# Kernel tuning notes

Measured on AMD Instinct MI355X. Metric: run time of the kernel, lower is better.

## Reference

```python
import jax, jax.numpy as jnp
import numpy as np

BATCH, PAST_N, HID, FEAT = 256, 512, 512, 1
INIT_MULT = 0.01  # ones * 0.01 initial state (perturb_init=False / eval mode)


def setup_inputs() -> dict:
    key = jax.random.key(0)
    ks = jax.random.split(key, 8)
    s = 1.0 / np.sqrt(HID)
    return {
        "input_seq": jax.random.normal(ks[0], (BATCH, PAST_N, FEAT), dtype=jnp.float32),
        "future_n": 64,
        "W_ih": jax.random.uniform(ks[1], (4 * HID, FEAT), minval=-s, maxval=s, dtype=jnp.float32),
        "W_hh": jax.random.uniform(ks[2], (4 * HID, HID), minval=-s, maxval=s, dtype=jnp.float32),
        "b_ih": jax.random.uniform(ks[3], (4 * HID,), minval=-s, maxval=s, dtype=jnp.float32),
        "b_hh": jax.random.uniform(ks[4], (4 * HID,), minval=-s, maxval=s, dtype=jnp.float32),
        "W_dec": jax.random.uniform(ks[5], (FEAT, HID), minval=-s, maxval=s, dtype=jnp.float32),
        "b_dec": jax.random.uniform(ks[6], (FEAT,), minval=-s, maxval=s, dtype=jnp.float32),
    }


def _lstm_cell(x, h, c, W_ih, W_hh, b_ih, b_hh):
    # PyTorch LSTMCell: gates ordered (i, f, g, o)
    gates = x @ W_ih.T + b_ih + h @ W_hh.T + b_hh  # [B, 4H]
    i, f, g, o = jnp.split(gates, 4, axis=-1)
    c_new = jax.nn.sigmoid(f) * c + jax.nn.sigmoid(i) * jnp.tanh(g)
    h_new = jax.nn.sigmoid(o) * jnp.tanh(c_new)
    return h_new, c_new


def reference(input_seq, future_n, W_ih, W_hh, b_ih, b_hh, W_dec, b_dec):
    B, T, _ = input_seq.shape
    h0 = jnp.full((B, HID), INIT_MULT, dtype=input_seq.dtype)
    c0 = jnp.full((B, HID), INIT_MULT, dtype=input_seq.dtype)

    xs = jnp.swapaxes(input_seq, 0, 1)  # [T, B, F]

    def past_step(carry, x_t):
        h, c = carry
        h, c = _lstm_cell(x_t, h, c, W_ih, W_hh, b_ih, b_hh)
        return (h, c), h

    (h, c), past_h = jax.lax.scan(past_step, (h0, c0), xs)  # past_h: [T, B, H]

    def future_step(carry, _):
        h, c = carry
        x_t = h @ W_dec.T + b_dec  # decode hidden -> next input, [B, F]
        h, c = _lstm_cell(x_t, h, c, W_ih, W_hh, b_ih, b_hh)
        return (h, c), h

    _, fut_h = jax.lax.scan(future_step, (h, c), None, length=future_n)  # [F_n, B, H]

    all_h = jnp.concatenate([past_h, fut_h], axis=0)  # [T+F_n, B, H]
    all_h = jnp.swapaxes(all_h, 0, 1)  # [B, T+F_n, H]
    return all_h @ W_dec.T + b_dec  # [B, T+F_n, 1]
```

## Files before the change

kernel.cpp:

```cpp
#include <hip/hip_runtime.h>
#include <hip/hip_fp16.h>


#define TPAST 512
#define TTOT  576
#define HIDN  512
#define BW    16
#define HW    64
#define NGRP  8
#define NWG   128
#define NTHR  512
#define HSTR  520
#define GSTR  261
#define BATCHN 256

typedef _Float16 half8   __attribute__((ext_vector_type(8)));
typedef _Float16 half2v  __attribute__((ext_vector_type(2)));
typedef float    float4v __attribute__((ext_vector_type(4)));
typedef int      int4v   __attribute__((ext_vector_type(4)));

__device__ __forceinline__ float fast_exp(float x) {
    return __builtin_amdgcn_exp2f(x * 1.44269504f);
}
__device__ __forceinline__ float fast_sigmoid(float x) {
    return __builtin_amdgcn_rcpf(1.0f + fast_exp(-x));
}
__device__ __forceinline__ float fast_tanh(float x) {
    return 1.0f - 2.0f * __builtin_amdgcn_rcpf(fast_exp(2.0f * x) + 1.0f);
}

__device__ __forceinline__ void ld32_sys(const void* p, int4v& a, int4v& b) {
    asm volatile("global_load_dwordx4 %0, %2, off sc0 sc1\n\t"
                 "global_load_dwordx4 %1, %2, off offset:16 sc0 sc1\n\t"
                 "s_waitcnt vmcnt(0)"
                 : "=v"(a), "=v"(b) : "v"(p) : "memory");
}
__device__ __forceinline__ void drain_vm() {
    asm volatile("s_waitcnt vmcnt(0)" ::: "memory");
}

__global__ __launch_bounds__(NTHR, 1)
void lstm_forecast_kernel(const float* __restrict__ xseq,
                          const float* __restrict__ Wih,
                          const float* __restrict__ Whh,
                          const float* __restrict__ bih,
                          const float* __restrict__ bhh,
                          const float* __restrict__ Wdec,
                          const float* __restrict__ bdec,
                          float* __restrict__ out,
                          unsigned int* __restrict__ flagbase,
                          unsigned int* __restrict__ hbuf)
{
    __shared__ _Float16 hcur[BW * HSTR];
    __shared__ float    gates[BW * GSTR];
    __shared__ float    wdecs[HIDN];
    __shared__ float    xcur[BW];

    const int tid  = threadIdx.x;
    const int bb   = blockIdx.x & 15;
    const int gb   = blockIdx.x >> 4;
    const int lane = tid & 63;
    const int wave = tid >> 6;
    const int m    = lane & 15;
    const int q    = lane >> 4;

    half8 Wf[2][16];
    {
        #pragma unroll
        for (int cbi = 0; cbi < 2; ++cbi) {
            const int col = (2 * wave + cbi) * 16 + m;
            const int gt  = col >> 6;
            const int jl  = col & 63;
            const float* wr = Whh + (size_t)(gt * HIDN + gb * HW + jl) * HIDN;
            #pragma unroll
            for (int kk = 0; kk < 16; ++kk) {
                const int k0 = kk * 32 + q * 8;
                float4v u = *(const float4v*)(wr + k0);
                float4v v = *(const float4v*)(wr + k0 + 4);
                half8 h;
                h[0] = (_Float16)u[0]; h[1] = (_Float16)u[1];
                h[2] = (_Float16)u[2]; h[3] = (_Float16)u[3];
                h[4] = (_Float16)v[0]; h[5] = (_Float16)v[1];
                h[6] = (_Float16)v[2]; h[7] = (_Float16)v[3];
                Wf[cbi][kk] = h;
            }
        }
    }

    const int eb = tid >> 5;
    const int jj = tid & 31;
    const int j0 = 2 * jj;
    float wih_r[2][4], bsum_r[2][4];
    #pragma unroll
    for (int p = 0; p < 2; ++p) {
        const int jg = gb * HW + j0 + p;
        #pragma unroll
        for (int gt = 0; gt < 4; ++gt) {
            const int r = gt * HIDN + jg;
            wih_r[p][gt]  = Wih[r];
            bsum_r[p][gt] = bih[r] + bhh[r];
        }
    }
    const float bdecv = bdec[0];
    float c0 = 0.01f, c1 = 0.01f;

    {
        const _Float16 hinit = (_Float16)0.01f;
        for (int i = tid; i < BW * HSTR; i += NTHR) hcur[i] = hinit;
        wdecs[tid] = Wdec[tid];
        if (tid < BW) xcur[tid] = xseq[(bb * BW + tid) * TPAST + 0];
    }
    __syncthreads();

    unsigned int* gflags = flagbase + bb * 16;
    const int bglob_e = bb * BW + eb;

    for (int t = 0; t < TTOT; ++t) {
        float4v acc0 = {0.f, 0.f, 0.f, 0.f};
        float4v acc1 = {0.f, 0.f, 0.f, 0.f};
        const _Float16* arow = hcur + m * HSTR + q * 8;
        #pragma unroll
        for (int kk = 0; kk < 16; ++kk) {
            half8 af = *(const half8*)(arow + kk * 32);
            acc0 = __builtin_amdgcn_mfma_f32_16x16x32_f16(af, Wf[0][kk], acc0, 0, 0, 0);
            acc1 = __builtin_amdgcn_mfma_f32_16x16x32_f16(af, Wf[1][kk], acc1, 0, 0, 0);
        }
        {
            const int colbase = wave * 32;
            #pragma unroll
            for (int r = 0; r < 4; ++r) {
                gates[(q * 4 + r) * GSTR + colbase +      m] = acc0[r];
                gates[(q * 4 + r) * GSTR + colbase + 16 + m] = acc1[r];
            }
        }
        const int tn = t + 1;
        float xq = 0.f;
        if (tn < TPAST && tid < BW) xq = xseq[(bb * BW + tid) * TPAST + tn];

        __syncthreads();

        {
            const float xc = xcur[eb];
            const float* grow = gates + eb * GSTR;

            float gi = grow[       j0] + xc * wih_r[0][0] + bsum_r[0][0];
            float gf = grow[ 64  + j0] + xc * wih_r[0][1] + bsum_r[0][1];
            float gg = grow[128  + j0] + xc * wih_r[0][2] + bsum_r[0][2];
            float go = grow[192  + j0] + xc * wih_r[0][3] + bsum_r[0][3];
            c0 = fast_sigmoid(gf) * c0 + fast_sigmoid(gi) * fast_tanh(gg);
            const float h0 = fast_sigmoid(go) * fast_tanh(c0);

            gi = grow[       j0 + 1] + xc * wih_r[1][0] + bsum_r[1][0];
            gf = grow[ 64  + j0 + 1] + xc * wih_r[1][1] + bsum_r[1][1];
            gg = grow[128  + j0 + 1] + xc * wih_r[1][2] + bsum_r[1][2];
            go = grow[192  + j0 + 1] + xc * wih_r[1][3] + bsum_r[1][3];
            c1 = fast_sigmoid(gf) * c1 + fast_sigmoid(gi) * fast_tanh(gg);
            const float h1 = fast_sigmoid(go) * fast_tanh(c1);

            half2v hp; hp[0] = (_Float16)h0; hp[1] = (_Float16)h1;
            const unsigned int bits = __builtin_bit_cast(unsigned int, hp);
            unsigned int* hdst = hbuf
                + (size_t)((tn & 1) * BATCHN + bglob_e) * (HIDN / 2)
                + gb * (HW / 2) + jj;
            __hip_atomic_store(hdst, bits, __ATOMIC_RELAXED,
                               __HIP_MEMORY_SCOPE_AGENT);
        }

        drain_vm();
        __syncthreads();

        const unsigned int target = (unsigned int)tn;
        if (tid == 0)
            __hip_atomic_store(gflags + gb, target, __ATOMIC_RELAXED,
                               __HIP_MEMORY_SCOPE_AGENT);
        {
            const unsigned int* slot = gflags + (lane & 7);
            int guard = 0;
            for (;;) {
                const unsigned int v = __hip_atomic_load(
                    slot, __ATOMIC_RELAXED, __HIP_MEMORY_SCOPE_AGENT);
                if (__ballot(v >= target) == ~0ull) break;
                __builtin_amdgcn_s_sleep(1);
                if (++guard > (1 << 22)) break;
            }
        }
        __builtin_amdgcn_sched_barrier(0);

        {
            const int p1 = tn & 1;
            const char* hsrc = (const char*)hbuf
                + ((size_t)(p1 * BATCHN + bb * BW)) * (HIDN * 2);
            const int row = 2 * wave + (lane >> 5);
            const int cb  = (lane & 31) * 32;
            int4v a, b;
            ld32_sys(hsrc + row * (HIDN * 2) + cb, a, b);
            _Float16* dst = hcur + row * HSTR + (lane & 31) * 16;
            *(int4v*)(dst)     = a;
            *(int4v*)(dst + 8) = b;
        }
        __syncthreads();

        if (wave < 2) {
            const int brow = 2 * gb + wave;
            const _Float16* hr = hcur + brow * HSTR + lane * 8;
            const float*    wr = wdecs + lane * 8;
            half8 hv = *(const half8*)hr;
            float dx = 0.f;
            #pragma unroll
            for (int e = 0; e < 8; ++e) dx += (float)hv[e] * wr[e];
            dx += __shfl_down(dx, 32);
            dx += __shfl_down(dx, 16);
            dx += __shfl_down(dx, 8);
            dx += __shfl_down(dx, 4);
            dx += __shfl_down(dx, 2);
            dx += __shfl_down(dx, 1);
            if (lane == 0)
                out[(bb * BW + brow) * TTOT + t] = dx + bdecv;
        }
        if (tn >= TPAST) {
            const _Float16* hr = hcur + eb * HSTR + jj * 16;
            const float*    wr = wdecs + jj * 16;
            float dx = 0.f;
            #pragma unroll
            for (int u = 0; u < 2; ++u) {
                half8 hv = *(const half8*)(hr + u * 8);
                #pragma unroll
                for (int e = 0; e < 8; ++e)
                    dx += (float)hv[e] * wr[u * 8 + e];
            }
            dx += __shfl_down(dx, 16);
            dx += __shfl_down(dx, 8);
            dx += __shfl_down(dx, 4);
            dx += __shfl_down(dx, 2);
            dx += __shfl_down(dx, 1);
            if ((lane & 31) == 0) xcur[eb] = dx + bdecv;
        } else {
            if (tid < BW) xcur[tid] = xq;
        }
    }
}

extern "C" void kernel_launch(void* const* d_in, const int* in_sizes, int n_in,
                              void* d_out, int out_size, void* d_ws, size_t ws_size,
                              hipStream_t stream) {
    (void)in_sizes; (void)n_in; (void)ws_size; (void)out_size;
    const float* xseq = (const float*)d_in[0];
    const float* Wih  = (const float*)d_in[2];
    const float* Whh  = (const float*)d_in[3];
    const float* bih  = (const float*)d_in[4];
    const float* bhh  = (const float*)d_in[5];
    const float* Wdec = (const float*)d_in[6];
    const float* bdec = (const float*)d_in[7];
    float* out = (float*)d_out;

    unsigned int* flags = (unsigned int*)d_ws;
    unsigned int* hbuf  = (unsigned int*)((char*)d_ws + 8192);

    hipMemsetAsync(d_ws, 0, 8192, stream);
    lstm_forecast_kernel<<<dim3(NWG), dim3(NTHR), 0, stream>>>(
        xseq, Wih, Whh, bih, bhh, Wdec, bdec, out, flags, hbuf);
}
```

Before: 1.662 ms.

## Use per-wave byte flags for grid sync and fuse decoder dot into h load

Replaces the per-workgroup flag, which needed a __syncthreads before one thread published it, with per-wave byte flags. Each wave publishes its own flag right after draining its stores and polls all 64 peer flags without sleeping, so one block-wide barrier per step goes away. The decoder dot product is now computed from the registers just loaded from the global h buffer, using Wdec held in registers, which removes a separate LDS pass and the shared Wdec array. The trade-offs are more flag traffic from 64 waves spinning, a wrapping 8-bit counter compared modulo 256, and a smaller spin guard.

```diff
diff --git a/kernel.cpp b/kernel.cpp
--- a/kernel.cpp
+++ b/kernel.cpp
@@ -35,6 +35,15 @@
                  "s_waitcnt vmcnt(0)"
                  : "=v"(a), "=v"(b) : "v"(p) : "memory");
 }
+__device__ __forceinline__ void st_byte_agent(unsigned char* p, unsigned int v) {
+    asm volatile("global_store_byte %0, %1, off sc1" :: "v"(p), "v"(v) : "memory");
+}
+__device__ __forceinline__ unsigned int ld_ubyte_agent(const unsigned char* p) {
+    unsigned int v;
+    asm volatile("global_load_ubyte %0, %1, off sc1\n\ts_waitcnt vmcnt(0)"
+                 : "=v"(v) : "v"(p) : "memory");
+    return v;
+}
 __device__ __forceinline__ void drain_vm() {
     asm volatile("s_waitcnt vmcnt(0)" ::: "memory");
 }
@@ -48,12 +57,11 @@
                           const float* __restrict__ Wdec,
                           const float* __restrict__ bdec,
                           float* __restrict__ out,
-                          unsigned int* __restrict__ flagbase,
+                          unsigned char* __restrict__ flagbase,
                           unsigned int* __restrict__ hbuf)
 {
     __shared__ _Float16 hcur[BW * HSTR];
     __shared__ float    gates[BW * GSTR];
-    __shared__ float    wdecs[HIDN];
     __shared__ float    xcur[BW];
 
     const int tid  = threadIdx.x;
@@ -101,21 +109,28 @@
             bsum_r[p][gt] = bih[r] + bhh[r];
         }
     }
+    float wdreg[16];
+    #pragma unroll
+    for (int e = 0; e < 16; ++e) wdreg[e] = Wdec[(lane & 31) * 16 + e];
     const float bdecv = bdec[0];
     float c0 = 0.01f, c1 = 0.01f;
 
     {
         const _Float16 hinit = (_Float16)0.01f;
         for (int i = tid; i < BW * HSTR; i += NTHR) hcur[i] = hinit;
-        wdecs[tid] = Wdec[tid];
         if (tid < BW) xcur[tid] = xseq[(bb * BW + tid) * TPAST + 0];
     }
     __syncthreads();
 
-    unsigned int* gflags = flagbase + bb * 16;
+    unsigned char* gflags = flagbase + bb * 128;
+    const int myidx = gb * 8 + wave;
     const int bglob_e = bb * BW + eb;
 
     for (int t = 0; t < TTOT; ++t) {
+        const int tn = t + 1;
+        float xq = 0.f;
+        if (tn < TPAST && tid < BW) xq = xseq[(bb * BW + tid) * TPAST + tn];
+
         float4v acc0 = {0.f, 0.f, 0.f, 0.f};
         float4v acc1 = {0.f, 0.f, 0.f, 0.f};
         const _Float16* arow = hcur + m * HSTR + q * 8;
@@ -133,10 +148,6 @@
                 gates[(q * 4 + r) * GSTR + colbase + 16 + m] = acc1[r];
             }
         }
-        const int tn = t + 1;
-        float xq = 0.f;
-        if (tn < TPAST && tid < BW) xq = xseq[(bb * BW + tid) * TPAST + tn];
-
         __syncthreads();
 
         {
@@ -167,76 +178,62 @@
         }
 
         drain_vm();
-        __syncthreads();
-
-        const unsigned int target = (unsigned int)tn;
-        if (tid == 0)
-            __hip_atomic_store(gflags + gb, target, __ATOMIC_RELAXED,
-                               __HIP_MEMORY_SCOPE_AGENT);
-        {
-            const unsigned int* slot = gflags + (lane & 7);
+        const unsigned int target8 = (unsigned int)tn & 0xffu;
+        if (lane == 0)
+            st_byte_agent(gflags + myidx, target8);
+        {
             int guard = 0;
             for (;;) {
-                const unsigned int v = __hip_atomic_load(
-                    slot, __ATOMIC_RELAXED, __HIP_MEMORY_SCOPE_AGENT);
-                if (__ballot(v >= target) == ~0ull) break;
-                __builtin_amdgcn_s_sleep(1);
-                if (++guard > (1 << 22)) break;
+                const unsigned int v = ld_ubyte_agent(gflags + lane);
+                const bool ok = (lane == myidx) || (((v - target8) & 0xffu) < 2u);
+                if (__ballot(ok) == ~0ull) break;
+                if (++guard > (1 << 19)) break;
             }
         }
         __builtin_amdgcn_sched_barrier(0);
 
+        int4v ra, rb;
         {
             const int p1 = tn & 1;
             const char* hsrc = (const char*)hbuf
                 + ((size_t)(p1 * BATCHN + bb * BW)) * (HIDN * 2);
             const int row = 2 * wave + (lane >> 5);
             const int cb  = (lane & 31) * 32;
-            int4v a, b;
-            ld32_sys(hsrc + row * (HIDN * 2) + cb, a, b);
+            ld32_sys(hsrc + row * (HIDN * 2) + cb, ra, rb);
             _Float16* dst = hcur + row * HSTR + (lane & 31) * 16;
-            *(int4v*)(dst)     = a;
-            *(int4v*)(dst + 8) = b;
+            *(int4v*)(dst)     = ra;
+            *(int4v*)(dst + 8) = rb;
+        }
+
+        {
+            const half8 ha = __builtin_bit_cast(half8, ra);
+            const half8 hb = __builtin_bit_cast(half8, rb);
+            float d = 0.f;
+            #pragma unroll
+            for (int e = 0; e < 8; ++e) d += (float)ha[e] * wdreg[e];
+            #pragma unroll
+            for (int e = 0; e < 8; ++e) d += (float)hb[e] * wdreg[8 + e];
+            d += __shfl_down(d, 16);
+            d += __shfl_down(d, 8);
+            d += __shfl_down(d, 4);
+            d += __shfl_down(d, 2);
+            d += __shfl_down(d, 1);
+            const float val = d + bdecv;
+
+            if (wave == gb) {
+                if (lane == 0)
+                    out[(bb * BW + 2 * gb    ) * TTOT + t] = val;
+                else if (lane == 32)
+                    out[(bb * BW + 2 * gb + 1) * TTOT + t] = val;
+            }
+            if (tn >= TPAST) {
+                if (lane == 0)       xcur[2 * wave    ] = val;
+                else if (lane == 32) xcur[2 * wave + 1] = val;
+            } else {
+                if (tid < BW) xcur[tid] = xq;
+            }
         }
         __syncthreads();
-
-        if (wave < 2) {
-            const int brow = 2 * gb + wave;
-            const _Float16* hr = hcur + brow * HSTR + lane * 8;
-            const float*    wr = wdecs + lane * 8;
-            half8 hv = *(const half8*)hr;
-            float dx = 0.f;
-            #pragma unroll
-            for (int e = 0; e < 8; ++e) dx += (float)hv[e] * wr[e];
-            dx += __shfl_down(dx, 32);
-            dx += __shfl_down(dx, 16);
-            dx += __shfl_down(dx, 8);
-            dx += __shfl_down(dx, 4);
-            dx += __shfl_down(dx, 2);
-            dx += __shfl_down(dx, 1);
-            if (lane == 0)
-                out[(bb * BW + brow) * TTOT + t] = dx + bdecv;
-        }
-        if (tn >= TPAST) {
-            const _Float16* hr = hcur + eb * HSTR + jj * 16;
-            const float*    wr = wdecs + jj * 16;
-            float dx = 0.f;
-            #pragma unroll
-            for (int u = 0; u < 2; ++u) {
-                half8 hv = *(const half8*)(hr + u * 8);
-                #pragma unroll
-                for (int e = 0; e < 8; ++e)
-                    dx += (float)hv[e] * wr[u * 8 + e];
-            }
-            dx += __shfl_down(dx, 16);
-            dx += __shfl_down(dx, 8);
-            dx += __shfl_down(dx, 4);
-            dx += __shfl_down(dx, 2);
-            dx += __shfl_down(dx, 1);
-            if ((lane & 31) == 0) xcur[eb] = dx + bdecv;
-        } else {
-            if (tid < BW) xcur[tid] = xq;
-        }
     }
 }
 
@@ -253,8 +250,8 @@
     const float* bdec = (const float*)d_in[7];
     float* out = (float*)d_out;
 
-    unsigned int* flags = (unsigned int*)d_ws;
-    unsigned int* hbuf  = (unsigned int*)((char*)d_ws + 8192);
+    unsigned char* flags = (unsigned char*)d_ws;
+    unsigned int*  hbuf  = (unsigned int*)((char*)d_ws + 8192);
 
     hipMemsetAsync(d_ws, 0, 8192, stream);
     lstm_forecast_kernel<<<dim3(NWG), dim3(NTHR), 0, stream>>>(
```

After: 3.034 ms. 82.5% more time.

## Interleave two batch sub-groups per workgroup to overlap barrier waits with compute

Applied to the files above, without the earlier changes.

Halves the grid to 64 workgroups. Each workgroup now processes two 16-row batch tiles (A and B) with staggered phases, so while one tile waits on the cross-workgroup flag barrier the other tile's MFMA and cell math run. This is meant to hide the per-step global synchronisation latency that dominates the sequential recurrence. In exchange each workgroup does twice the work per step and uses more LDS and more complex flag ordering, which risks correctness or deadlock if the phase ordering is wrong.

```diff
diff --git a/kernel.cpp b/kernel.cpp
--- a/kernel.cpp
+++ b/kernel.cpp
@@ -7,8 +7,7 @@
 #define HIDN  512
 #define BW    16
 #define HW    64
-#define NGRP  8
-#define NWG   128
+#define NWG   64
 #define NTHR  512
 #define HSTR  520
 #define GSTR  261
@@ -51,18 +50,22 @@
                           unsigned int* __restrict__ flagbase,
                           unsigned int* __restrict__ hbuf)
 {
-    __shared__ _Float16 hcur[BW * HSTR];
+    __shared__ _Float16 hcurA[BW * HSTR];
+    __shared__ _Float16 hcurB[BW * HSTR];
     __shared__ float    gates[BW * GSTR];
     __shared__ float    wdecs[HIDN];
-    __shared__ float    xcur[BW];
+    __shared__ float    xcurA[BW];
+    __shared__ float    xcurB[BW];
 
     const int tid  = threadIdx.x;
-    const int bb   = blockIdx.x & 15;
-    const int gb   = blockIdx.x >> 4;
+    const int sg   = blockIdx.x & 7;
+    const int gb   = blockIdx.x >> 3;
     const int lane = tid & 63;
     const int wave = tid >> 6;
     const int m    = lane & 15;
     const int q    = lane >> 4;
+    const int baseA = sg * 32;
+    const int baseB = sg * 32 + 16;
 
     half8 Wf[2][16];
     {
@@ -102,123 +105,114 @@
         }
     }
     const float bdecv = bdec[0];
-    float c0 = 0.01f, c1 = 0.01f;
-
+    float cA0 = 0.01f, cA1 = 0.01f, cB0 = 0.01f, cB1 = 0.01f;
+
+    float xqA = 0.f, xqB = 0.f;
     {
         const _Float16 hinit = (_Float16)0.01f;
-        for (int i = tid; i < BW * HSTR; i += NTHR) hcur[i] = hinit;
+        for (int i = tid; i < BW * HSTR; i += NTHR) { hcurA[i] = hinit; hcurB[i] = hinit; }
         wdecs[tid] = Wdec[tid];
-        if (tid < BW) xcur[tid] = xseq[(bb * BW + tid) * TPAST + 0];
+        if (tid < BW) {
+            xqA = xseq[(baseA + tid) * TPAST + 0];
+            xqB = xseq[(baseB + tid) * TPAST + 0];
+        }
     }
     __syncthreads();
 
-    unsigned int* gflags = flagbase + bb * 16;
-    const int bglob_e = bb * BW + eb;
-
-    for (int t = 0; t < TTOT; ++t) {
-        float4v acc0 = {0.f, 0.f, 0.f, 0.f};
-        float4v acc1 = {0.f, 0.f, 0.f, 0.f};
-        const _Float16* arow = hcur + m * HSTR + q * 8;
+    unsigned int* flagsA = flagbase + sg * 64;
+    unsigned int* flagsB = flagsA + 32;
+
+    auto mfma_stage = [&](const _Float16* hc) {
+        float4v a0 = {0.f, 0.f, 0.f, 0.f};
+        float4v a1 = {0.f, 0.f, 0.f, 0.f};
+        const _Float16* arow = hc + m * HSTR + q * 8;
         #pragma unroll
         for (int kk = 0; kk < 16; ++kk) {
             half8 af = *(const half8*)(arow + kk * 32);
-            acc0 = __builtin_amdgcn_mfma_f32_16x16x32_f16(af, Wf[0][kk], acc0, 0, 0, 0);
-            acc1 = __builtin_amdgcn_mfma_f32_16x16x32_f16(af, Wf[1][kk], acc1, 0, 0, 0);
-        }
-        {
-            const int colbase = wave * 32;
-            #pragma unroll
-            for (int r = 0; r < 4; ++r) {
-                gates[(q * 4 + r) * GSTR + colbase +      m] = acc0[r];
-                gates[(q * 4 + r) * GSTR + colbase + 16 + m] = acc1[r];
-            }
-        }
-        const int tn = t + 1;
-        float xq = 0.f;
-        if (tn < TPAST && tid < BW) xq = xseq[(bb * BW + tid) * TPAST + tn];
-
-        __syncthreads();
-
-        {
-            const float xc = xcur[eb];
-            const float* grow = gates + eb * GSTR;
-
-            float gi = grow[       j0] + xc * wih_r[0][0] + bsum_r[0][0];
-            float gf = grow[ 64  + j0] + xc * wih_r[0][1] + bsum_r[0][1];
-            float gg = grow[128  + j0] + xc * wih_r[0][2] + bsum_r[0][2];
-            float go = grow[192  + j0] + xc * wih_r[0][3] + bsum_r[0][3];
-            c0 = fast_sigmoid(gf) * c0 + fast_sigmoid(gi) * fast_tanh(gg);
-            const float h0 = fast_sigmoid(go) * fast_tanh(c0);
-
-            gi = grow[       j0 + 1] + xc * wih_r[1][0] + bsum_r[1][0];
-            gf = grow[ 64  + j0 + 1] + xc * wih_r[1][1] + bsum_r[1][1];
-            gg = grow[128  + j0 + 1] + xc * wih_r[1][2] + bsum_r[1][2];
-            go = grow[192  + j0 + 1] + xc * wih_r[1][3] + bsum_r[1][3];
-            c1 = fast_sigmoid(gf) * c1 + fast_sigmoid(gi) * fast_tanh(gg);
-            const float h1 = fast_sigmoid(go) * fast_tanh(c1);
-
-            half2v hp; hp[0] = (_Float16)h0; hp[1] = (_Float16)h1;
-            const unsigned int bits = __builtin_bit_cast(unsigned int, hp);
-            unsigned int* hdst = hbuf
-                + (size_t)((tn & 1) * BATCHN + bglob_e) * (HIDN / 2)
-                + gb * (HW / 2) + jj;
-            __hip_atomic_store(hdst, bits, __ATOMIC_RELAXED,
-                               __HIP_MEMORY_SCOPE_AGENT);
-        }
-
-        drain_vm();
-        __syncthreads();
-
-        const unsigned int target = (unsigned int)tn;
-        if (tid == 0)
-            __hip_atomic_store(gflags + gb, target, __ATOMIC_RELAXED,
-                               __HIP_MEMORY_SCOPE_AGENT);
-        {
-            const unsigned int* slot = gflags + (lane & 7);
-            int guard = 0;
-            for (;;) {
-                const unsigned int v = __hip_atomic_load(
-                    slot, __ATOMIC_RELAXED, __HIP_MEMORY_SCOPE_AGENT);
-                if (__ballot(v >= target) == ~0ull) break;
-                __builtin_amdgcn_s_sleep(1);
-                if (++guard > (1 << 22)) break;
-            }
+            a0 = __builtin_amdgcn_mfma_f32_16x16x32_f16(af, Wf[0][kk], a0, 0, 0, 0);
+            a1 = __builtin_amdgcn_mfma_f32_16x16x32_f16(af, Wf[1][kk], a1, 0, 0, 0);
+        }
+        const int colbase = wave * 32;
+        #pragma unroll
+        for (int r = 0; r < 4; ++r) {
+            gates[(q * 4 + r) * GSTR + colbase +      m] = a0[r];
+            gates[(q * 4 + r) * GSTR + colbase + 16 + m] = a1[r];
+        }
+    };
+
+    auto cell_store = [&](const float* xc, float& c0, float& c1,
+                          int growbase, int par) {
+        const float xcv = xc[eb];
+        const float* grow = gates + eb * GSTR;
+
+        float gi = grow[       j0] + xcv * wih_r[0][0] + bsum_r[0][0];
+        float gf = grow[ 64  + j0] + xcv * wih_r[0][1] + bsum_r[0][1];
+        float gg = grow[128  + j0] + xcv * wih_r[0][2] + bsum_r[0][2];
+        float go = grow[192  + j0] + xcv * wih_r[0][3] + bsum_r[0][3];
+        c0 = fast_sigmoid(gf) * c0 + fast_sigmoid(gi) * fast_tanh(gg);
+        const float h0 = fast_sigmoid(go) * fast_tanh(c0);
+
+        gi = grow[       j0 + 1] + xcv * wih_r[1][0] + bsum_r[1][0];
+        gf = grow[ 64  + j0 + 1] + xcv * wih_r[1][1] + bsum_r[1][1];
+        gg = grow[128  + j0 + 1] + xcv * wih_r[1][2] + bsum_r[1][2];
+        go = grow[192  + j0 + 1] + xcv * wih_r[1][3] + bsum_r[1][3];
+        c1 = fast_sigmoid(gf) * c1 + fast_sigmoid(gi) * fast_tanh(gg);
+        const float h1 = fast_sigmoid(go) * fast_tanh(c1);
+
+        half2v hp; hp[0] = (_Float16)h0; hp[1] = (_Float16)h1;
+        const unsigned int bits = __builtin_bit_cast(unsigned int, hp);
+        unsigned int* hdst = hbuf
+            + (size_t)(par * BATCHN + growbase + eb) * (HIDN / 2)
+            + gb * (HW / 2) + jj;
+        __hip_atomic_store(hdst, bits, __ATOMIC_RELAXED,
+                           __HIP_MEMORY_SCOPE_AGENT);
+    };
+
+    auto poll = [&](const unsigned int* line, unsigned int target) {
+        const unsigned int* slot = line + (lane & 7);
+        int guard = 0;
+        for (;;) {
+            const unsigned int v = __hip_atomic_load(
+                slot, __ATOMIC_RELAXED, __HIP_MEMORY_SCOPE_AGENT);
+            if (__ballot(v >= target) == ~0ull) break;
+            __builtin_amdgcn_s_sleep(1);
+            if (++guard > (1 << 22)) break;
         }
         __builtin_amdgcn_sched_barrier(0);
-
-        {
-            const int p1 = tn & 1;
-            const char* hsrc = (const char*)hbuf
-                + ((size_t)(p1 * BATCHN + bb * BW)) * (HIDN * 2);
-            const int row = 2 * wave + (lane >> 5);
-            const int cb  = (lane & 31) * 32;
-            int4v a, b;
-            ld32_sys(hsrc + row * (HIDN * 2) + cb, a, b);
-            _Float16* dst = hcur + row * HSTR + (lane & 31) * 16;
-            *(int4v*)(dst)     = a;
-            *(int4v*)(dst + 8) = b;
-        }
-        __syncthreads();
-
+    };
+
+    auto reload = [&](_Float16* hc, int growbase, int par) {
+        const char* hsrc = (const char*)hbuf
+            + ((size_t)(par * BATCHN + growbase)) * (HIDN * 2);
+        const int row = 2 * wave + (lane >> 5);
+        const int cb  = (lane & 31) * 32;
+        int4v a, b;
+        ld32_sys(hsrc + row * (HIDN * 2) + cb, a, b);
+        _Float16* dst = hc + row * HSTR + (lane & 31) * 16;
+        *(int4v*)(dst)     = a;
+        *(int4v*)(dst + 8) = b;
+    };
+
+    auto decode = [&](const _Float16* hc, float* xc, int growbase,
+                      int t_out, bool dofuture) {
         if (wave < 2) {
             const int brow = 2 * gb + wave;
-            const _Float16* hr = hcur + brow * HSTR + lane * 8;
-            const float*    wr = wdecs + lane * 8;
-            half8 hv = *(const half8*)hr;
-            float dx = 0.f;
+            half8 hv = *(const half8*)(hc + brow * HSTR + lane * 8);
+            const float* wr = wdecs + lane * 8;
+            float d = 0.f;
             #pragma unroll
-            for (int e = 0; e < 8; ++e) dx += (float)hv[e] * wr[e];
-            dx += __shfl_down(dx, 32);
-            dx += __shfl_down(dx, 16);
-            dx += __shfl_down(dx, 8);
-            dx += __shfl_down(dx, 4);
-            dx += __shfl_down(dx, 2);
-            dx += __shfl_down(dx, 1);
+            for (int e = 0; e < 8; ++e) d += (float)hv[e] * wr[e];
+            d += __shfl_down(d, 32);
+            d += __shfl_down(d, 16);
+            d += __shfl_down(d, 8);
+            d += __shfl_down(d, 4);
+            d += __shfl_down(d, 2);
+            d += __shfl_down(d, 1);
             if (lane == 0)
-                out[(bb * BW + brow) * TTOT + t] = dx + bdecv;
-        }
-        if (tn >= TPAST) {
-            const _Float16* hr = hcur + eb * HSTR + jj * 16;
+                out[(growbase + brow) * TTOT + t_out] = d + bdecv;
+        }
+        if (dofuture) {
+            const _Float16* hr = hc + eb * HSTR + jj * 16;
             const float*    wr = wdecs + jj * 16;
             float dx = 0.f;
             #pragma unroll
@@ -233,11 +227,59 @@
             dx += __shfl_down(dx, 4);
             dx += __shfl_down(dx, 2);
             dx += __shfl_down(dx, 1);
-            if ((lane & 31) == 0) xcur[eb] = dx + bdecv;
-        } else {
-            if (tid < BW) xcur[tid] = xq;
-        }
+            if ((lane & 31) == 0) xc[eb] = dx + bdecv;
+        }
+    };
+
+    for (int t = 0; t < TTOT; ++t) {
+        const int tp1 = t + 1;
+        const int par = tp1 & 1;
+
+        if (tid < BW) {
+            if (t < TPAST)  { xcurA[tid] = xqA; xcurB[tid] = xqB; }
+            if (tp1 < TPAST) {
+                xqA = xseq[(baseA + tid) * TPAST + tp1];
+                xqB = xseq[(baseB + tid) * TPAST + tp1];
+            }
+        }
+
+        mfma_stage(hcurA);
+        __syncthreads();
+        cell_store(xcurA, cA0, cA1, baseA, par);
+        __syncthreads();
+
+        mfma_stage(hcurB);
+        if (t > 0) poll(flagsB, (unsigned int)t);
+        drain_vm();
+        __syncthreads();
+        if (tid == 0)
+            __hip_atomic_store(flagsA + gb, (unsigned int)tp1,
+                               __ATOMIC_RELAXED, __HIP_MEMORY_SCOPE_AGENT);
+
+        if (t > 0) {
+            reload(hcurB, baseB, t & 1);
+            __syncthreads();
+            decode(hcurB, xcurB, baseB, t - 1, t >= TPAST);
+        }
+
+        cell_store(xcurB, cB0, cB1, baseB, par);
+
+        poll(flagsA, (unsigned int)tp1);
+        drain_vm();
+        __syncthreads();
+        if (tid == 0)
+            __hip_atomic_store(flagsB + gb, (unsigned int)tp1,
+                               __ATOMIC_RELAXED, __HIP_MEMORY_SCOPE_AGENT);
+
+        reload(hcurA, baseA, par);
+        __syncthreads();
+        decode(hcurA, xcurA, baseA, t, tp1 >= TPAST);
     }
+
+    poll(flagsB, (unsigned int)TTOT);
+    reload(hcurB, baseB, TTOT & 1);
+    __syncthreads();
+    decode(hcurB, xcurB, baseB, TTOT - 1, false);
 }
 
 extern "C" void kernel_launch(void* const* d_in, const int* in_sizes, int n_in,
```

Result: slower. 2.409 ms (+44.9%).

## Replace flag barrier with step-tagged hidden-state packets polled directly

Applied to the files above, without the earlier changes.

Each hidden-state pair is now published as a 64-bit packet carrying the step number alongside the fp16 data. Consumers poll the data itself until every tag matches the current step. This removes the separate flag store, the vmem drain, one workgroup barrier and the extra load round-trip after the flag wait. In exchange, global traffic per step doubles, and the workspace memset is dropped, so tags left over from an earlier launch could be mistaken for fresh data.

```diff
diff --git a/kernel.cpp b/kernel.cpp
--- a/kernel.cpp
+++ b/kernel.cpp
@@ -7,17 +7,16 @@
 #define HIDN  512
 #define BW    16
 #define HW    64
-#define NGRP  8
 #define NWG   128
 #define NTHR  512
 #define HSTR  520
+#define HSTR32 260
 #define GSTR  261
 #define BATCHN 256
 
 typedef _Float16 half8   __attribute__((ext_vector_type(8)));
 typedef _Float16 half2v  __attribute__((ext_vector_type(2)));
 typedef float    float4v __attribute__((ext_vector_type(4)));
-typedef int      int4v   __attribute__((ext_vector_type(4)));
 
 __device__ __forceinline__ float fast_exp(float x) {
     return __builtin_amdgcn_exp2f(x * 1.44269504f);
@@ -29,14 +28,24 @@
     return 1.0f - 2.0f * __builtin_amdgcn_rcpf(fast_exp(2.0f * x) + 1.0f);
 }
 
-__device__ __forceinline__ void ld32_sys(const void* p, int4v& a, int4v& b) {
-    asm volatile("global_load_dwordx4 %0, %2, off sc0 sc1\n\t"
-                 "global_load_dwordx4 %1, %2, off offset:16 sc0 sc1\n\t"
-                 "s_waitcnt vmcnt(0)"
-                 : "=v"(a), "=v"(b) : "v"(p) : "memory");
-}
-__device__ __forceinline__ void drain_vm() {
-    asm volatile("s_waitcnt vmcnt(0)" ::: "memory");
+__device__ __forceinline__ void ld8x8_sys(const void* p,
+        unsigned long long& v0, unsigned long long& v1,
+        unsigned long long& v2, unsigned long long& v3,
+        unsigned long long& v4, unsigned long long& v5,
+        unsigned long long& v6, unsigned long long& v7) {
+    asm volatile(
+        "global_load_dwordx2 %0, %8, off sc0 sc1\n\t"
+        "global_load_dwordx2 %1, %8, off offset:512 sc0 sc1\n\t"
+        "global_load_dwordx2 %2, %8, off offset:1024 sc0 sc1\n\t"
+        "global_load_dwordx2 %3, %8, off offset:1536 sc0 sc1\n\t"
+        "global_load_dwordx2 %4, %8, off offset:2048 sc0 sc1\n\t"
+        "global_load_dwordx2 %5, %8, off offset:2560 sc0 sc1\n\t"
+        "global_load_dwordx2 %6, %8, off offset:3072 sc0 sc1\n\t"
+        "global_load_dwordx2 %7, %8, off offset:3584 sc0 sc1\n\t"
+        "s_waitcnt vmcnt(0)"
+        : "=v"(v0), "=v"(v1), "=v"(v2), "=v"(v3),
+          "=v"(v4), "=v"(v5), "=v"(v6), "=v"(v7)
+        : "v"(p) : "memory");
 }
 
 __global__ __launch_bounds__(NTHR, 1)
@@ -48,8 +57,7 @@
                           const float* __restrict__ Wdec,
                           const float* __restrict__ bdec,
                           float* __restrict__ out,
-                          unsigned int* __restrict__ flagbase,
-                          unsigned int* __restrict__ hbuf)
+                          unsigned long long* __restrict__ hbuf64)
 {
     __shared__ _Float16 hcur[BW * HSTR];
     __shared__ float    gates[BW * GSTR];
@@ -112,8 +120,8 @@
     }
     __syncthreads();
 
-    unsigned int* gflags = flagbase + bb * 16;
     const int bglob_e = bb * BW + eb;
+    unsigned int* hc32 = (unsigned int*)hcur;
 
     for (int t = 0; t < TTOT; ++t) {
         float4v acc0 = {0.f, 0.f, 0.f, 0.f};
@@ -134,6 +142,7 @@
             }
         }
         const int tn = t + 1;
+        const int par = tn & 1;
         float xq = 0.f;
         if (tn < TPAST && tid < BW) xq = xseq[(bb * BW + tid) * TPAST + tn];
 
@@ -159,63 +168,62 @@
 
             half2v hp; hp[0] = (_Float16)h0; hp[1] = (_Float16)h1;
             const unsigned int bits = __builtin_bit_cast(unsigned int, hp);
-            unsigned int* hdst = hbuf
-                + (size_t)((tn & 1) * BATCHN + bglob_e) * (HIDN / 2)
-                + gb * (HW / 2) + jj;
-            __hip_atomic_store(hdst, bits, __ATOMIC_RELAXED,
-                               __HIP_MEMORY_SCOPE_AGENT);
-        }
-
-        drain_vm();
-        __syncthreads();
-
-        const unsigned int target = (unsigned int)tn;
-        if (tid == 0)
-            __hip_atomic_store(gflags + gb, target, __ATOMIC_RELAXED,
-                               __HIP_MEMORY_SCOPE_AGENT);
+            const unsigned long long pkt =
+                ((unsigned long long)(unsigned int)tn << 32) |
+                (unsigned long long)bits;
+            __hip_atomic_store(hbuf64
+                    + (size_t)(par * BATCHN + bglob_e) * 256 + gb * 32 + jj,
+                pkt, __ATOMIC_RELAXED, __HIP_MEMORY_SCOPE_AGENT);
+        }
+
         {
-            const unsigned int* slot = gflags + (lane & 7);
+            const unsigned long long* base = hbuf64
+                + (size_t)(par * BATCHN + bb * BW + 2 * wave) * 256 + lane;
+            unsigned long long v0, v1, v2, v3, v4, v5, v6, v7;
+            const unsigned int want = (unsigned int)tn;
             int guard = 0;
             for (;;) {
-                const unsigned int v = __hip_atomic_load(
-                    slot, __ATOMIC_RELAXED, __HIP_MEMORY_SCOPE_AGENT);
-                if (__ballot(v >= target) == ~0ull) break;
+                ld8x8_sys(base, v0, v1, v2, v3, v4, v5, v6, v7);
+                bool ok = ((unsigned int)(v0 >> 32) == want)
+                        & ((unsigned int)(v1 >> 32) == want)
+                        & ((unsigned int)(v2 >> 32) == want)
+                        & ((unsigned int)(v3 >> 32) == want)
+                        & ((unsigned int)(v4 >> 32) == want)
+                        & ((unsigned int)(v5 >> 32) == want)
+                        & ((unsigned int)(v6 >> 32) == want)
+                        & ((unsigned int)(v7 >> 32) == want);
+                if (__ballot(ok) == ~0ull) break;
                 __builtin_amdgcn_s_sleep(1);
-                if (++guard > (1 << 22)) break;
-            }
-        }
-        __builtin_amdgcn_sched_barrier(0);
-
-        {
-            const int p1 = tn & 1;
-            const char* hsrc = (const char*)hbuf
-                + ((size_t)(p1 * BATCHN + bb * BW)) * (HIDN * 2);
-            const int row = 2 * wave + (lane >> 5);
-            const int cb  = (lane & 31) * 32;
-            int4v a, b;
-            ld32_sys(hsrc + row * (HIDN * 2) + cb, a, b);
-            _Float16* dst = hcur + row * HSTR + (lane & 31) * 16;
-            *(int4v*)(dst)     = a;
-            *(int4v*)(dst + 8) = b;
+                if (++guard > (1 << 20)) break;
+            }
+            __builtin_amdgcn_sched_barrier(0);
+            const int r0 = 2 * wave * HSTR32 + lane;
+            hc32[r0          ] = (unsigned int)v0;
+            hc32[r0 +  64    ] = (unsigned int)v1;
+            hc32[r0 + 128    ] = (unsigned int)v2;
+            hc32[r0 + 192    ] = (unsigned int)v3;
+            hc32[r0 + HSTR32      ] = (unsigned int)v4;
+            hc32[r0 + HSTR32 +  64] = (unsigned int)v5;
+            hc32[r0 + HSTR32 + 128] = (unsigned int)v6;
+            hc32[r0 + HSTR32 + 192] = (unsigned int)v7;
         }
         __syncthreads();
 
         if (wave < 2) {
             const int brow = 2 * gb + wave;
-            const _Float16* hr = hcur + brow * HSTR + lane * 8;
-            const float*    wr = wdecs + lane * 8;
-            half8 hv = *(const half8*)hr;
-            float dx = 0.f;
-            #pragma unroll
-            for (int e = 0; e < 8; ++e) dx += (float)hv[e] * wr[e];
-            dx += __shfl_down(dx, 32);
-            dx += __shfl_down(dx, 16);
-            dx += __shfl_down(dx, 8);
-            dx += __shfl_down(dx, 4);
-            dx += __shfl_down(dx, 2);
-            dx += __shfl_down(dx, 1);
+            half8 hv = *(const half8*)(hcur + brow * HSTR + lane * 8);
+            const float* wr = wdecs + lane * 8;
+            float d = 0.f;
+            #pragma unroll
+            for (int e = 0; e < 8; ++e) d += (float)hv[e] * wr[e];
+            d += __shfl_down(d, 32);
+            d += __shfl_down(d, 16);
+            d += __shfl_down(d, 8);
+            d += __shfl_down(d, 4);
+            d += __shfl_down(d, 2);
+            d += __shfl_down(d, 1);
             if (lane == 0)
-                out[(bb * BW + brow) * TTOT + t] = dx + bdecv;
+                out[(bb * BW + brow) * TTOT + t] = d + bdecv;
         }
         if (tn >= TPAST) {
             const _Float16* hr = hcur + eb * HSTR + jj * 16;
@@ -253,10 +261,8 @@
     const float* bdec = (const float*)d_in[7];
     float* out = (float*)d_out;
 
-    unsigned int* flags = (unsigned int*)d_ws;
-    unsigned int* hbuf  = (unsigned int*)((char*)d_ws + 8192);
-
-    hipMemsetAsync(d_ws, 0, 8192, stream);
+    unsigned long long* hbuf64 = (unsigned long long*)d_ws;
+
     lstm_forecast_kernel<<<dim3(NWG), dim3(NTHR), 0, stream>>>(
-        xseq, Wih, Whh, bih, bhh, Wdec, bdec, out, flags, hbuf);
-}
+        xseq, Wih, Whh, bih, bhh, Wdec, bdec, out, hbuf64);
+}
```

After: 1.699 ms. +2.2%, slower.
